# Performance work log

Measured on AMD Instinct MI355X. Metric: run time of the kernel, lower is better.

## Reference

```python
import jax, jax.numpy as jnp
import numpy as np

N, E = 50000, 800000
NFEAT, NHID, NHEADS, NCLASS = 512, 64, 8, 64
ALPHA = 0.2  # leaky relu negative slope


def setup_inputs() -> dict:
    key = jax.random.key(0)
    ks = jax.random.split(key, 8)
    x = jax.random.normal(ks[0], (N, NFEAT), jnp.float32)
    row = jax.random.randint(ks[1], (E,), 0, N)  # destination node i of each edge
    col = jax.random.randint(ks[2], (E,), 0, N)  # source node j of each edge
    W = jax.random.normal(ks[3], (NHEADS, NFEAT, NHID), jnp.float32) * (1.0 / np.sqrt(NFEAT))
    a = jax.random.normal(ks[4], (NHEADS, 2 * NHID), jnp.float32) * 0.1
    W_out = jax.random.normal(ks[5], (NHID * NHEADS, NCLASS), jnp.float32) * (1.0 / np.sqrt(NHID * NHEADS))
    a_out = jax.random.normal(ks[6], (2 * NCLASS,), jnp.float32) * 0.1
    return {"x": x, "row": row, "col": col, "W": W, "a": a, "W_out": W_out, "a_out": a_out}


def _gat_layer(h, W, a, row, col, n, alpha, concat):
    # h: [N, F_in], W: [F_in, F'], a: [2*F']
    Wh = h @ W                                   # [N, F']
    f = Wh.shape[-1]
    f_dst = Wh @ a[:f]                           # a^T part for target node i, [N]
    f_src = Wh @ a[f:]                           # a^T part for source node j, [N]
    e = jax.nn.leaky_relu(f_dst[row] + f_src[col], alpha)       # [E] attention logits
    # numerically stable segment softmax over incoming edges of each node
    m = jax.ops.segment_max(e, row, num_segments=n)
    m = jnp.where(jnp.isneginf(m), 0.0, m)       # nodes with no in-edges
    p = jnp.exp(e - m[row])
    denom = jax.ops.segment_sum(p, row, num_segments=n)
    att = p / jnp.maximum(denom[row], 1e-16)     # [E]
    out = jax.ops.segment_sum(att[:, None] * Wh[col], row, num_segments=n)  # [N, F']
    return jax.nn.elu(out) if concat else out


def reference(x, row, col, W, a, W_out, a_out):
    # eval mode: F.dropout is a no-op
    heads = [_gat_layer(x, W[h], a[h], row, col, N, ALPHA, True) for h in range(NHEADS)]
    h = jnp.concatenate(heads, axis=1)           # [N, NHID*NHEADS]
    return _gat_layer(h, W_out, a_out, row, col, N, ALPHA, False)  # [N, NCLASS]
```

## Files before the change

### kernel.cpp

```cpp
#include <hip/hip_runtime.h>
#include <cstdint>
#include <cstddef>

#define NN      50000
#define MPAD    50048
#define EE      800000
#define NHEADS  8
#define HID_TOT 512
#define NCLASS  64
#define ALPHA_LRELU 0.2f
#define NB1     196
#define CAP1    128
#define CAP2    128

typedef unsigned short u16;
typedef __attribute__((ext_vector_type(8))) unsigned short ushort8;

__device__ __forceinline__ float bf2f(u16 v) {
    return __uint_as_float(((unsigned)v) << 16);
}
__device__ __forceinline__ u16 f2bf(float f) {
    unsigned u = __float_as_uint(f);
    return (u16)((u + 0x7fffu + ((u >> 16) & 1u)) >> 16);
}


__global__ void fill_i32(int* __restrict__ p, int v, long n) {
    long i = (long)blockIdx.x * blockDim.x + threadIdx.x;
    if (i < n) p[i] = v;
}
__global__ void fill_u16(u16* __restrict__ p, u16 v, long n) {
    long i = (long)blockIdx.x * blockDim.x + threadIdx.x;
    if (i < n) p[i] = v;
}

__global__ void cast_x(const float* __restrict__ x, u16* __restrict__ xb) {
    int g = blockIdx.x * 256 + threadIdx.x;
    if (g >= MPAD * 64) return;
    int r = g >> 6;
    int c = (g & 63) * 8;
    ushort8 o = (ushort8)0;
    if (r < NN) {
        const float4 v0 = *(const float4*)(x + (size_t)r * 512 + c);
        const float4 v1 = *(const float4*)(x + (size_t)r * 512 + c + 4);
        o[0] = f2bf(v0.x); o[1] = f2bf(v0.y); o[2] = f2bf(v0.z); o[3] = f2bf(v0.w);
        o[4] = f2bf(v1.x); o[5] = f2bf(v1.y); o[6] = f2bf(v1.z); o[7] = f2bf(v1.w);
    }
    *(ushort8*)(xb + (size_t)r * 512 + c) = o;
}

__global__ void pack_w1t(const float* __restrict__ W, u16* __restrict__ Wt) {
    int idx = blockIdx.x * 256 + threadIdx.x;
    if (idx >= 512 * 512) return;
    int c = idx >> 9, f = idx & 511;
    int h = c >> 6, j = c & 63;
    Wt[idx] = f2bf(W[(h << 15) + (f << 6) + j]);
}

__global__ void pack_woutt(const float* __restrict__ W, u16* __restrict__ Wt) {
    int idx = blockIdx.x * 256 + threadIdx.x;
    if (idx >= 64 * 512) return;
    int n = idx >> 9, k = idx & 511;
    Wt[idx] = f2bf(W[k * 64 + n]);
}


__global__ void hist_rows(const int* __restrict__ row, int* __restrict__ cnt) {
    int e = blockIdx.x * 256 + threadIdx.x;
    if (e >= EE) return;
    atomicAdd(&cnt[row[e]], 1);
}

__global__ __launch_bounds__(256) void scan_blocksum(const int* __restrict__ cnt,
                                                     int* __restrict__ bsum) {
    int idx = blockIdx.x * 256 + threadIdx.x;
    int v = (idx < NN) ? cnt[idx] : 0;
    #pragma unroll
    for (int o = 32; o; o >>= 1) v += __shfl_xor(v, o);
    __shared__ int sw[4];
    int wave = threadIdx.x >> 6;
    if ((threadIdx.x & 63) == 0) sw[wave] = v;
    __syncthreads();
    if (threadIdx.x == 0) bsum[blockIdx.x] = sw[0] + sw[1] + sw[2] + sw[3];
}

__global__ __launch_bounds__(256) void scan_bsums(const int* __restrict__ bsum,
                                                  int* __restrict__ boff) {
    __shared__ int sh[256];
    int t = threadIdx.x;
    int v = (t < NB1) ? bsum[t] : 0;
    sh[t] = v;
    __syncthreads();
    for (int o = 1; o < 256; o <<= 1) {
        int cur = sh[t];
        int add = (t >= o) ? sh[t - o] : 0;
        __syncthreads();
        sh[t] = cur + add;
        __syncthreads();
    }
    if (t < NB1) boff[t] = sh[t] - v;
}

__global__ __launch_bounds__(256) void scan_write(const int* __restrict__ cnt,
                                                  const int* __restrict__ boff,
                                                  int* __restrict__ start,
                                                  int* __restrict__ wr) {
    __shared__ int sh[256];
    int t = threadIdx.x;
    int idx = blockIdx.x * 256 + t;
    int c = (idx < NN) ? cnt[idx] : 0;
    sh[t] = c;
    __syncthreads();
    for (int o = 1; o < 256; o <<= 1) {
        int cur = sh[t];
        int add = (t >= o) ? sh[t - o] : 0;
        __syncthreads();
        sh[t] = cur + add;
        __syncthreads();
    }
    if (idx < NN) {
        int excl = boff[blockIdx.x] + sh[t] - c;
        start[idx] = excl;
        wr[idx] = excl;
    }
    if (idx == 0) start[NN] = EE;
}

__global__ void scatter_edges(const int* __restrict__ row, const int* __restrict__ col,
                              int* __restrict__ wr, int* __restrict__ ecol) {
    int e = blockIdx.x * 256 + threadIdx.x;
    if (e >= EE) return;
    int i = row[e];
    int pos = atomicAdd(&wr[i], 1);
    ecol[pos] = col[e];
}


__device__ __forceinline__ void load_lds_128(const u16* g, u16* l) {
    __builtin_amdgcn_global_load_lds((const __attribute__((address_space(1))) void*)g,
                                     (__attribute__((address_space(3))) void*)l,
                                     16, 0, 0);
}

typedef __attribute__((ext_vector_type(8))) short frag8;
typedef __attribute__((ext_vector_type(4))) float f32x4;

template <int BN, int OUT_MODE>
__global__ __launch_bounds__(256) void gemm_bf16(const u16* __restrict__ A,
                                                 const u16* __restrict__ Bt,
                                                 void* __restrict__ Cv,
                                                 int M, int N, int K) {
    constexpr int BM = 128, BK = 32;
    constexpr int WN = BN / 2;
    constexpr int NT = WN / 16;
    __shared__ u16 As[BM * BK];
    __shared__ u16 Bs[BN * BK];
    const int tid = threadIdx.x;
    const int wave = tid >> 6, lane = tid & 63;
    const int wm = wave & 1, wn = wave >> 1;
    const int bm = blockIdx.y * BM, bn = blockIdx.x * BN;
    const int q = lane >> 4, lr = lane & 15;

    f32x4 acc[4][NT] = {};

    for (int k0 = 0; k0 < K; k0 += BK) {
        #pragma unroll
        for (int c = wave; c < (BM * BK) / 512; c += 4) {
            int f = c * 512 + lane * 8;
            int row = f >> 5, ck = f & 31;
            load_lds_128(A + (size_t)(bm + row) * K + k0 + ck, As + c * 512);
        }
        #pragma unroll
        for (int c = wave; c < (BN * BK) / 512; c += 4) {
            int f = c * 512 + lane * 8;
            int row = f >> 5, ck = f & 31;
            load_lds_128(Bt + (size_t)(bn + row) * K + k0 + ck, Bs + c * 512);
        }
        __syncthreads();
        frag8 af[4], bfr[NT];
        #pragma unroll
        for (int am = 0; am < 4; am++)
            af[am] = *(const frag8*)(As + (wm * 64 + am * 16 + lr) * 32 + q * 8);
        #pragma unroll
        for (int bt = 0; bt < NT; bt++)
            bfr[bt] = *(const frag8*)(Bs + (wn * WN + bt * 16 + lr) * 32 + q * 8);
        #pragma unroll
        for (int am = 0; am < 4; am++)
            #pragma unroll
            for (int bt = 0; bt < NT; bt++)
                acc[am][bt] = __builtin_amdgcn_mfma_f32_16x16x32_bf16(af[am], bfr[bt], acc[am][bt], 0, 0, 0);
        __syncthreads();
    }

    #pragma unroll
    for (int am = 0; am < 4; am++) {
        #pragma unroll
        for (int reg = 0; reg < 4; reg++) {
            int gr = bm + wm * 64 + am * 16 + q * 4 + reg;
            if (gr < M) {
                #pragma unroll
                for (int bt = 0; bt < NT; bt++) {
                    int gc = bn + wn * WN + bt * 16 + lr;
                    float v = acc[am][bt][reg];
                    if (OUT_MODE == 0) ((float*)Cv)[(size_t)gr * N + gc] = v;
                    else               ((u16*)Cv)[(size_t)gr * N + gc] = f2bf(v);
                }
            }
        }
    }
}

__global__ __launch_bounds__(256) void dots1(const u16* __restrict__ Wh, const float* __restrict__ a,
                                             float* __restrict__ fd, float* __restrict__ fs) {
    __shared__ float as[8 * 128];
    for (int k = threadIdx.x; k < 8 * 128; k += 256) as[k] = a[k];
    __syncthreads();
    int idx = blockIdx.x * 256 + threadIdx.x;
    if (idx >= NN * NHEADS) return;
    int n = idx >> 3, h = idx & 7;
    const u16* w = Wh + (size_t)n * HID_TOT + h * 64;
    const float* ad = as + h * 128;
    float sd = 0.f, ss = 0.f;
    #pragma unroll
    for (int c = 0; c < 8; c++) {
        ushort8 v8 = *(const ushort8*)(w + c * 8);
        #pragma unroll
        for (int k = 0; k < 8; k++) {
            float v = bf2f(v8[k]);
            sd += v * ad[c * 8 + k];
            ss += v * ad[64 + c * 8 + k];
        }
    }
    fd[idx] = sd;
    fs[idx] = ss;
}

__global__ __launch_bounds__(256) void dots2(const u16* __restrict__ Wh2b, const float* __restrict__ a_out,
                                             float* __restrict__ fd, float* __restrict__ fs) {
    __shared__ float as[128];
    if (threadIdx.x < 128) as[threadIdx.x] = a_out[threadIdx.x];
    __syncthreads();
    int n = blockIdx.x * 256 + threadIdx.x;
    if (n >= NN) return;
    const u16* w = Wh2b + (size_t)n * NCLASS;
    float sd = 0.f, ss = 0.f;
    #pragma unroll
    for (int c = 0; c < 8; c++) {
        ushort8 v8 = *(const ushort8*)(w + c * 8);
        #pragma unroll
        for (int k = 0; k < 8; k++) {
            float v = bf2f(v8[k]);
            sd += v * as[c * 8 + k];
            ss += v * as[64 + c * 8 + k];
        }
    }
    fd[n] = sd;
    fs[n] = ss;
}

__global__ __launch_bounds__(256) void agg1_fused(const int* __restrict__ start,
                                                  const int* __restrict__ ecol,
                                                  const float* __restrict__ fd,
                                                  const float* __restrict__ fs,
                                                  const u16* __restrict__ Whb,
                                                  u16* __restrict__ h1b) {
    __shared__ float vc[4][CAP1 * 8];
    const int w = threadIdx.x >> 6;
    const int i = blockIdx.x * 4 + w;
    const int lane = threadIdx.x & 63;
    const int g = lane >> 3, h = lane & 7;
    const int st = start[i], en = start[i + 1];

    const float fdv1 = fd[i * 8 + h];
    float m = -__builtin_huge_valf();
    for (int t = st + g; t < en; t += 8) {
        int j = ecol[t];
        float v = fdv1 + fs[j * 8 + h];
        v = v > 0.f ? v : ALPHA_LRELU * v;
        int c = t - st;
        if (c < CAP1) vc[w][c * 8 + h] = v;
        m = fmaxf(m, v);
    }
    m = fmaxf(m, __shfl_xor(m, 8));
    m = fmaxf(m, __shfl_xor(m, 16));
    m = fmaxf(m, __shfl_xor(m, 32));
    __syncthreads();

    const int hh = lane >> 3;
    const float mh = __shfl(m, hh);
    const float fdv2 = fd[i * 8 + hh];
    float acc[8] = {};
    float den = 0.f;
    for (int t = st; t < en; ++t) {
        int c = t - st;
        float v;
        if (c < CAP1) {
            v = vc[w][c * 8 + hh];
        } else {
            int jj = ecol[t];
            v = fdv2 + fs[jj * 8 + hh];
            v = v > 0.f ? v : ALPHA_LRELU * v;
        }
        float p = __expf(v - mh);
        den += p;
        int j = ecol[t];
        ushort8 wv = *(const ushort8*)(Whb + (size_t)j * HID_TOT + lane * 8);
        #pragma unroll
        for (int k = 0; k < 8; k++) acc[k] += p * bf2f(wv[k]);
    }
    float rden = 1.0f / fmaxf(den, 1e-16f);
    ushort8 o8;
    #pragma unroll
    for (int k = 0; k < 8; k++) {
        float v = acc[k] * rden;
        v = v > 0.f ? v : (__expf(v) - 1.0f);
        o8[k] = f2bf(v);
    }
    *(ushort8*)(h1b + (size_t)i * HID_TOT + lane * 8) = o8;
}

__global__ __launch_bounds__(256) void agg2_fused(const int* __restrict__ start,
                                                  const int* __restrict__ ecol,
                                                  const float* __restrict__ fd,
                                                  const float* __restrict__ fs,
                                                  const u16* __restrict__ Wh2b,
                                                  float* __restrict__ out) {
    __shared__ float vc[4][CAP2];
    const int w = threadIdx.x >> 6;
    const int i = blockIdx.x * 4 + w;
    const int lane = threadIdx.x & 63;
    const int st = start[i], en = start[i + 1];
    const float fdv = fd[i];

    float m = -__builtin_huge_valf();
    for (int t = st + lane; t < en; t += 64) {
        int j = ecol[t];
        float v = fdv + fs[j];
        v = v > 0.f ? v : ALPHA_LRELU * v;
        int c = t - st;
        if (c < CAP2) vc[w][c] = v;
        m = fmaxf(m, v);
    }
    #pragma unroll
    for (int o = 32; o; o >>= 1) m = fmaxf(m, __shfl_xor(m, o));
    __syncthreads();

    float acc = 0.f, den = 0.f;
    for (int t = st; t < en; ++t) {
        int c = t - st;
        float v;
        if (c < CAP2) {
            v = vc[w][c];
        } else {
            int jj = ecol[t];
            v = fdv + fs[jj];
            v = v > 0.f ? v : ALPHA_LRELU * v;
        }
        float p = __expf(v - m);
        den += p;
        int j = ecol[t];
        acc += p * bf2f(Wh2b[(size_t)j * NCLASS + lane]);
    }
    out[(size_t)i * NCLASS + lane] = acc / fmaxf(den, 1e-16f);
}


static inline int cdiv_l(long a, long b) { return (int)((a + b - 1) / b); }

extern "C" void kernel_launch(void* const* d_in, const int* in_sizes, int n_in,
                              void* d_out, int out_size, void* d_ws, size_t ws_size,
                              hipStream_t stream) {
    const float* x     = (const float*)d_in[0];
    const int*   row   = (const int*)d_in[1];
    const int*   col   = (const int*)d_in[2];
    const float* W     = (const float*)d_in[3];
    const float* a     = (const float*)d_in[4];
    const float* W_out = (const float*)d_in[5];
    const float* a_out = (const float*)d_in[6];
    float* out = (float*)d_out;

    char* wsb = (char*)d_ws;
    size_t off = 0;
    auto alloc = [&](size_t bytes) { char* p = wsb + off; off += (bytes + 255) & ~(size_t)255; return p; };
    u16*   xb     = (u16*)  alloc((size_t)MPAD * 512 * 2);
    u16*   Wcat_t = (u16*)  alloc((size_t)512 * 512 * 2);
    u16*   Wot_t  = (u16*)  alloc((size_t)64 * 512 * 2);
    u16*   Whb1   = (u16*)  alloc((size_t)NN * 512 * 2);
    float* fd1    = (float*)alloc((size_t)NN * 8 * 4);
    float* fs1    = (float*)alloc((size_t)NN * 8 * 4);
    u16*   h1b    = (u16*)  alloc((size_t)MPAD * 512 * 2);
    u16*   Wh2b   = (u16*)  alloc((size_t)NN * 64 * 2);
    float* fd2    = (float*)alloc((size_t)NN * 4);
    float* fs2    = (float*)alloc((size_t)NN * 4);
    int*   cnt    = (int*)  alloc((size_t)NN * 4);
    int*   startp = (int*)  alloc(((size_t)NN + 1) * 4);
    int*   wr     = (int*)  alloc((size_t)NN * 4);
    int*   ecol   = (int*)  alloc((size_t)EE * 4);
    int*   bsum   = (int*)  alloc((size_t)NB1 * 4);
    int*   boff   = (int*)  alloc((size_t)NB1 * 4);

    fill_i32<<<cdiv_l(NN, 256), 256, 0, stream>>>(cnt, 0, (long)NN);
    hist_rows<<<cdiv_l(EE, 256), 256, 0, stream>>>(row, cnt);
    scan_blocksum<<<NB1, 256, 0, stream>>>(cnt, bsum);
    scan_bsums<<<1, 256, 0, stream>>>(bsum, boff);
    scan_write<<<NB1, 256, 0, stream>>>(cnt, boff, startp, wr);
    scatter_edges<<<cdiv_l(EE, 256), 256, 0, stream>>>(row, col, wr, ecol);

    cast_x<<<cdiv_l((long)MPAD * 64, 256), 256, 0, stream>>>(x, xb);
    pack_w1t<<<cdiv_l(512 * 512, 256), 256, 0, stream>>>(W, Wcat_t);
    pack_woutt<<<cdiv_l(64 * 512, 256), 256, 0, stream>>>(W_out, Wot_t);
    fill_u16<<<cdiv_l((long)(MPAD - NN) * 512, 256), 256, 0, stream>>>(
        h1b + (size_t)NN * 512, 0, (long)(MPAD - NN) * 512);

    {
        dim3 grid(512 / 128, cdiv_l(MPAD, 128));
        gemm_bf16<128, 1><<<grid, 256, 0, stream>>>(xb, Wcat_t, Whb1, NN, 512, 512);
    }
    dots1<<<cdiv_l((long)NN * 8, 256), 256, 0, stream>>>(Whb1, a, fd1, fs1);
    agg1_fused<<<NN / 4, 256, 0, stream>>>(startp, ecol, fd1, fs1, Whb1, h1b);

    {
        dim3 grid(1, cdiv_l(MPAD, 128));
        gemm_bf16<64, 1><<<grid, 256, 0, stream>>>(h1b, Wot_t, Wh2b, NN, 64, 512);
    }
    dots2<<<cdiv_l(NN, 256), 256, 0, stream>>>(Wh2b, a_out, fd2, fs2);
    agg2_fused<<<NN / 4, 256, 0, stream>>>(startp, ecol, fd2, fs2, Wh2b, out);
}
```

Baseline: 556.6 us.

## Fuse prep kernels, fold attention dots into GEMM epilogue, restructure aggregations

Merges the four preparation kernels (x cast, two weight packs, pad fill) into one launch. The first-layer attention dot products are now computed in the GEMM epilogue from fp32 accumulators via 16-lane shuffles, which removes the separate dots1 pass over Wh. The layer-1 aggregation loop is unrolled by two edges to overlap gathers. The layer-2 aggregation splits each wave into four edge groups with 4-wide vector loads, followed by a cross-group shuffle reduction. The dots now use unrounded fp32 values instead of bf16-rounded ones, which slightly changes numerics.

After: 493.3 us. -11.4%, faster.

```diff
diff --git a/kernel.cpp b/kernel.cpp
--- a/kernel.cpp
+++ b/kernel.cpp
@@ -15,6 +15,7 @@
 
 typedef unsigned short u16;
 typedef __attribute__((ext_vector_type(8))) unsigned short ushort8;
+typedef __attribute__((ext_vector_type(4))) unsigned short ushort4v;
 
 __device__ __forceinline__ float bf2f(u16 v) {
     return __uint_as_float(((unsigned)v) << 16);
@@ -24,46 +25,57 @@
     return (u16)((u + 0x7fffu + ((u >> 16) & 1u)) >> 16);
 }
 
+#define PREP_R0 (MPAD * 64)
+#define PREP_R1 (512 * 512)
+#define PREP_R2 (64 * 512)
+#define PREP_R3 ((MPAD - NN) * 64)
+#define PREP_TOT (PREP_R0 + PREP_R1 + PREP_R2 + PREP_R3)
+
+__global__ __launch_bounds__(256) void prep_all(const float* __restrict__ x,
+                                                const float* __restrict__ W,
+                                                const float* __restrict__ W_out,
+                                                u16* __restrict__ xb,
+                                                u16* __restrict__ Wt1,
+                                                u16* __restrict__ Wto,
+                                                u16* __restrict__ h1b) {
+    int g = blockIdx.x * 256 + threadIdx.x;
+    if (g < PREP_R0) {
+        int r = g >> 6;
+        int c = (g & 63) * 8;
+        ushort8 o = (ushort8)0;
+        if (r < NN) {
+            const float4 v0 = *(const float4*)(x + (size_t)r * 512 + c);
+            const float4 v1 = *(const float4*)(x + (size_t)r * 512 + c + 4);
+            o[0] = f2bf(v0.x); o[1] = f2bf(v0.y); o[2] = f2bf(v0.z); o[3] = f2bf(v0.w);
+            o[4] = f2bf(v1.x); o[5] = f2bf(v1.y); o[6] = f2bf(v1.z); o[7] = f2bf(v1.w);
+        }
+        *(ushort8*)(xb + (size_t)r * 512 + c) = o;
+        return;
+    }
+    g -= PREP_R0;
+    if (g < PREP_R1) {
+        int c = g >> 9, f = g & 511;
+        int h = c >> 6, j = c & 63;
+        Wt1[g] = f2bf(W[(h << 15) + (f << 6) + j]);
+        return;
+    }
+    g -= PREP_R1;
+    if (g < PREP_R2) {
+        int n = g >> 9, k = g & 511;
+        Wto[g] = f2bf(W_out[k * 64 + n]);
+        return;
+    }
+    g -= PREP_R2;
+    if (g < PREP_R3) {
+        *(ushort8*)(h1b + (size_t)NN * 512 + (size_t)g * 8) = (ushort8)0;
+    }
+}
+
 
 __global__ void fill_i32(int* __restrict__ p, int v, long n) {
     long i = (long)blockIdx.x * blockDim.x + threadIdx.x;
     if (i < n) p[i] = v;
 }
-__global__ void fill_u16(u16* __restrict__ p, u16 v, long n) {
-    long i = (long)blockIdx.x * blockDim.x + threadIdx.x;
-    if (i < n) p[i] = v;
-}
-
-__global__ void cast_x(const float* __restrict__ x, u16* __restrict__ xb) {
-    int g = blockIdx.x * 256 + threadIdx.x;
-    if (g >= MPAD * 64) return;
-    int r = g >> 6;
-    int c = (g & 63) * 8;
-    ushort8 o = (ushort8)0;
-    if (r < NN) {
-        const float4 v0 = *(const float4*)(x + (size_t)r * 512 + c);
-        const float4 v1 = *(const float4*)(x + (size_t)r * 512 + c + 4);
-        o[0] = f2bf(v0.x); o[1] = f2bf(v0.y); o[2] = f2bf(v0.z); o[3] = f2bf(v0.w);
-        o[4] = f2bf(v1.x); o[5] = f2bf(v1.y); o[6] = f2bf(v1.z); o[7] = f2bf(v1.w);
-    }
-    *(ushort8*)(xb + (size_t)r * 512 + c) = o;
-}
-
-__global__ void pack_w1t(const float* __restrict__ W, u16* __restrict__ Wt) {
-    int idx = blockIdx.x * 256 + threadIdx.x;
-    if (idx >= 512 * 512) return;
-    int c = idx >> 9, f = idx & 511;
-    int h = c >> 6, j = c & 63;
-    Wt[idx] = f2bf(W[(h << 15) + (f << 6) + j]);
-}
-
-__global__ void pack_woutt(const float* __restrict__ W, u16* __restrict__ Wt) {
-    int idx = blockIdx.x * 256 + threadIdx.x;
-    if (idx >= 64 * 512) return;
-    int n = idx >> 9, k = idx & 511;
-    Wt[idx] = f2bf(W[k * 64 + n]);
-}
-
 
 __global__ void hist_rows(const int* __restrict__ row, int* __restrict__ cnt) {
     int e = blockIdx.x * 256 + threadIdx.x;
@@ -145,11 +157,14 @@
 typedef __attribute__((ext_vector_type(8))) short frag8;
 typedef __attribute__((ext_vector_type(4))) float f32x4;
 
-template <int BN, int OUT_MODE>
+template <int BN, int OUT_MODE, bool FUSE_DOTS>
 __global__ __launch_bounds__(256) void gemm_bf16(const u16* __restrict__ A,
                                                  const u16* __restrict__ Bt,
                                                  void* __restrict__ Cv,
-                                                 int M, int N, int K) {
+                                                 int M, int N, int K,
+                                                 const float* __restrict__ av,
+                                                 float* __restrict__ fd,
+                                                 float* __restrict__ fs) {
     constexpr int BM = 128, BK = 32;
     constexpr int WN = BN / 2;
     constexpr int NT = WN / 16;
@@ -192,12 +207,25 @@
         __syncthreads();
     }
 
+    float adv[NT], adv2[NT];
+    int hd = 0;
+    if (FUSE_DOTS) {
+        hd = blockIdx.x * 2 + wn;
+        const float* ah = av + hd * 128;
+        #pragma unroll
+        for (int bt = 0; bt < NT; bt++) {
+            adv[bt]  = ah[bt * 16 + lr];
+            adv2[bt] = ah[64 + bt * 16 + lr];
+        }
+    }
+
     #pragma unroll
     for (int am = 0; am < 4; am++) {
         #pragma unroll
         for (int reg = 0; reg < 4; reg++) {
             int gr = bm + wm * 64 + am * 16 + q * 4 + reg;
-            if (gr < M) {
+            bool inb = gr < M;
+            if (inb) {
                 #pragma unroll
                 for (int bt = 0; bt < NT; bt++) {
                     int gc = bn + wn * WN + bt * 16 + lr;
@@ -206,34 +234,28 @@
                     else               ((u16*)Cv)[(size_t)gr * N + gc] = f2bf(v);
                 }
             }
-        }
-    }
-}
-
-__global__ __launch_bounds__(256) void dots1(const u16* __restrict__ Wh, const float* __restrict__ a,
-                                             float* __restrict__ fd, float* __restrict__ fs) {
-    __shared__ float as[8 * 128];
-    for (int k = threadIdx.x; k < 8 * 128; k += 256) as[k] = a[k];
-    __syncthreads();
-    int idx = blockIdx.x * 256 + threadIdx.x;
-    if (idx >= NN * NHEADS) return;
-    int n = idx >> 3, h = idx & 7;
-    const u16* w = Wh + (size_t)n * HID_TOT + h * 64;
-    const float* ad = as + h * 128;
-    float sd = 0.f, ss = 0.f;
-    #pragma unroll
-    for (int c = 0; c < 8; c++) {
-        ushort8 v8 = *(const ushort8*)(w + c * 8);
-        #pragma unroll
-        for (int k = 0; k < 8; k++) {
-            float v = bf2f(v8[k]);
-            sd += v * ad[c * 8 + k];
-            ss += v * ad[64 + c * 8 + k];
-        }
-    }
-    fd[idx] = sd;
-    fs[idx] = ss;
-}
+            if (FUSE_DOTS) {
+                float sd = 0.f, ss = 0.f;
+                #pragma unroll
+                for (int bt = 0; bt < NT; bt++) {
+                    float v = acc[am][bt][reg];
+                    sd += v * adv[bt];
+                    ss += v * adv2[bt];
+                }
+                #pragma unroll
+                for (int o = 1; o < 16; o <<= 1) {
+                    sd += __shfl_xor(sd, o);
+                    ss += __shfl_xor(ss, o);
+                }
+                if (lr == 0 && inb) {
+                    fd[gr * 8 + hd] = sd;
+                    fs[gr * 8 + hd] = ss;
+                }
+            }
+        }
+    }
+}
+
 
 __global__ __launch_bounds__(256) void dots2(const u16* __restrict__ Wh2b, const float* __restrict__ a_out,
                                              float* __restrict__ fd, float* __restrict__ fs) {
@@ -291,19 +313,36 @@
     const float fdv2 = fd[i * 8 + hh];
     float acc[8] = {};
     float den = 0.f;
-    for (int t = st; t < en; ++t) {
+    int t = st;
+    for (; t + 2 <= en; t += 2) {
+        int c0 = t - st, c1 = c0 + 1;
+        int j0 = ecol[t], j1 = ecol[t + 1];
+        float v0, v1;
+        if (c1 < CAP1) {
+            v0 = vc[w][c0 * 8 + hh];
+            v1 = vc[w][c1 * 8 + hh];
+        } else {
+            v0 = fdv2 + fs[j0 * 8 + hh]; v0 = v0 > 0.f ? v0 : ALPHA_LRELU * v0;
+            v1 = fdv2 + fs[j1 * 8 + hh]; v1 = v1 > 0.f ? v1 : ALPHA_LRELU * v1;
+        }
+        float p0 = __expf(v0 - mh);
+        float p1 = __expf(v1 - mh);
+        den += p0 + p1;
+        ushort8 w0 = *(const ushort8*)(Whb + (size_t)j0 * HID_TOT + lane * 8);
+        ushort8 w1 = *(const ushort8*)(Whb + (size_t)j1 * HID_TOT + lane * 8);
+        #pragma unroll
+        for (int k = 0; k < 8; k++) acc[k] += p0 * bf2f(w0[k]);
+        #pragma unroll
+        for (int k = 0; k < 8; k++) acc[k] += p1 * bf2f(w1[k]);
+    }
+    if (t < en) {
         int c = t - st;
+        int j = ecol[t];
         float v;
-        if (c < CAP1) {
-            v = vc[w][c * 8 + hh];
-        } else {
-            int jj = ecol[t];
-            v = fdv2 + fs[jj * 8 + hh];
-            v = v > 0.f ? v : ALPHA_LRELU * v;
-        }
+        if (c < CAP1) v = vc[w][c * 8 + hh];
+        else { v = fdv2 + fs[j * 8 + hh]; v = v > 0.f ? v : ALPHA_LRELU * v; }
         float p = __expf(v - mh);
         den += p;
-        int j = ecol[t];
         ushort8 wv = *(const ushort8*)(Whb + (size_t)j * HID_TOT + lane * 8);
         #pragma unroll
         for (int k = 0; k < 8; k++) acc[k] += p * bf2f(wv[k]);
@@ -345,8 +384,10 @@
     for (int o = 32; o; o >>= 1) m = fmaxf(m, __shfl_xor(m, o));
     __syncthreads();
 
-    float acc = 0.f, den = 0.f;
-    for (int t = st; t < en; ++t) {
+    const int g = lane >> 4, r = lane & 15;
+    float acc[4] = {};
+    float den = 0.f;
+    for (int t = st + g; t < en; t += 4) {
         int c = t - st;
         float v;
         if (c < CAP2) {
@@ -359,9 +400,23 @@
         float p = __expf(v - m);
         den += p;
         int j = ecol[t];
-        acc += p * bf2f(Wh2b[(size_t)j * NCLASS + lane]);
-    }
-    out[(size_t)i * NCLASS + lane] = acc / fmaxf(den, 1e-16f);
+        ushort4v wv = *(const ushort4v*)(Wh2b + (size_t)j * NCLASS + r * 4);
+        #pragma unroll
+        for (int k = 0; k < 4; k++) acc[k] += p * bf2f(wv[k]);
+    }
+    #pragma unroll
+    for (int o = 16; o <= 32; o <<= 1) {
+        den += __shfl_xor(den, o);
+        #pragma unroll
+        for (int k = 0; k < 4; k++) acc[k] += __shfl_xor(acc[k], o);
+    }
+    if (g == 0) {
+        float rden = 1.0f / fmaxf(den, 1e-16f);
+        float4 o4;
+        o4.x = acc[0] * rden; o4.y = acc[1] * rden;
+        o4.z = acc[2] * rden; o4.w = acc[3] * rden;
+        *(float4*)(out + (size_t)i * NCLASS + r * 4) = o4;
+    }
 }
 
 
@@ -406,22 +461,19 @@
     scan_write<<<NB1, 256, 0, stream>>>(cnt, boff, startp, wr);
     scatter_edges<<<cdiv_l(EE, 256), 256, 0, stream>>>(row, col, wr, ecol);
 
-    cast_x<<<cdiv_l((long)MPAD * 64, 256), 256, 0, stream>>>(x, xb);
-    pack_w1t<<<cdiv_l(512 * 512, 256), 256, 0, stream>>>(W, Wcat_t);
-    pack_woutt<<<cdiv_l(64 * 512, 256), 256, 0, stream>>>(W_out, Wot_t);
-    fill_u16<<<cdiv_l((long)(MPAD - NN) * 512, 256), 256, 0, stream>>>(
-        h1b + (size_t)NN * 512, 0, (long)(MPAD - NN) * 512);
+    prep_all<<<cdiv_l(PREP_TOT, 256), 256, 0, stream>>>(x, W, W_out, xb, Wcat_t, Wot_t, h1b);
 
     {
         dim3 grid(512 / 128, cdiv_l(MPAD, 128));
-        gemm_bf16<128, 1><<<grid, 256, 0, stream>>>(xb, Wcat_t, Whb1, NN, 512, 512);
-    }
-    dots1<<<cdiv_l((long)NN * 8, 256), 256, 0, stream>>>(Whb1, a, fd1, fs1);
+        gemm_bf16<128, 1, true><<<grid, 256, 0, stream>>>(xb, Wcat_t, Whb1, NN, 512, 512,
+                                                          a, fd1, fs1);
+    }
     agg1_fused<<<NN / 4, 256, 0, stream>>>(startp, ecol, fd1, fs1, Whb1, h1b);
 
     {
         dim3 grid(1, cdiv_l(MPAD, 128));
-        gemm_bf16<64, 1><<<grid, 256, 0, stream>>>(h1b, Wot_t, Wh2b, NN, 64, 512);
+        gemm_bf16<64, 1, false><<<grid, 256, 0, stream>>>(h1b, Wot_t, Wh2b, NN, 64, 512,
+                                                          nullptr, nullptr, nullptr);
     }
     dots2<<<cdiv_l(NN, 256), 256, 0, stream>>>(Wh2b, a_out, fd2, fs2);
     agg2_fused<<<NN / 4, 256, 0, stream>>>(startp, ecol, fd2, fs2, Wh2b, out);
```
